# Kernel optimization log

Hardware: AMD Instinct MI355X
Metric: run time of the kernel (lower is better)

The kernel has to match this reference:

```python
import jax, jax.numpy as jnp
import numpy as np

B, S, D, NB = 8, 8192, 512, 16


def _ln(x, g, b, eps=1e-5):
    m = jnp.mean(x, axis=-1, keepdims=True)
    v = jnp.var(x, axis=-1, keepdims=True)
    return (x - m) / jnp.sqrt(v + eps) * g + b


def setup_inputs() -> dict:
    key = jax.random.key(0)
    ks = jax.random.split(key, 12)
    s = 0.02
    f32 = jnp.float32
    return {
        "emb_input": jax.random.normal(ks[0], (B, S, D), f32),
        "dis_input": jax.random.normal(ks[1], (B, S, D), f32),
        "torsion": jax.random.normal(ks[2], (B, D), f32),
        "dis_unlocked": 1,
        "delay_steps": 3,
        # embodied selector + per-block params (stacked over NB blocks)
        "emb_sel_W": jax.random.normal(ks[3], (D, NB), f32) * s,
        "emb_sel_b": jnp.zeros((NB,), f32),
        "emb_ln_g": jnp.ones((NB, D), f32),
        "emb_ln_b": jnp.zeros((NB, D), f32),
        "emb_w1": jax.random.normal(ks[4], (NB, D, D), f32) * s,
        "emb_b1": jnp.zeros((NB, D), f32),
        "emb_w2": jax.random.normal(ks[5], (NB, D, D), f32) * s,
        "emb_b2": jnp.zeros((NB, D), f32),
        # disembodied selector + per-block params
        "dis_sel_W": jax.random.normal(ks[6], (D, NB), f32) * s,
        "dis_sel_b": jnp.zeros((NB,), f32),
        "dis_ln1_g": jnp.ones((NB, D), f32),
        "dis_ln1_b": jnp.zeros((NB, D), f32),
        "dis_attn_W": jax.random.normal(ks[7], (NB, D, D), f32) * s,
        "dis_attn_b": jnp.zeros((NB, D), f32),
        "dis_ln2_g": jnp.ones((NB, D), f32),
        "dis_ln2_b": jnp.zeros((NB, D), f32),
        "dis_ff1_W": jax.random.normal(ks[8], (NB, D, 2 * D), f32) * s,
        "dis_ff1_b": jnp.zeros((NB, 2 * D), f32),
        "dis_ff2_W": jax.random.normal(ks[9], (NB, 2 * D, D), f32) * s,
        "dis_ff2_b": jnp.zeros((NB, D), f32),
    }


def reference(emb_input, dis_input, torsion, dis_unlocked, delay_steps,
              emb_sel_W, emb_sel_b, emb_ln_g, emb_ln_b, emb_w1, emb_b1, emb_w2, emb_b2,
              dis_sel_W, dis_sel_b, dis_ln1_g, dis_ln1_b, dis_attn_W, dis_attn_b,
              dis_ln2_g, dis_ln2_b, dis_ff1_W, dis_ff1_b, dis_ff2_W, dis_ff2_b):
    # ---- embodied branch: sigmoid-gated top-2 routing (indices from batch elem 0)
    scores = jax.nn.sigmoid(jnp.mean(emb_input, axis=1) @ emb_sel_W + emb_sel_b)  # [B,NB]
    _, top = jax.lax.top_k(scores[0], 2)
    t_emb = 1.0 + torsion[:, None, :] * 0.1  # [B,1,D]
    h = emb_input
    for i in range(2):  # fixed top-2, unrolled; block params gathered dynamically
        idx = top[i]
        hn = _ln(h, emb_ln_g[idx], emb_ln_b[idx])
        hn = jnp.tanh(hn @ emb_w1[idx] + emb_b1[idx]) @ emb_w2[idx] + emb_b2[idx]
        h = h + hn * t_emb * 0.3
    emb_h = h

    # ---- disembodied branch (dis_unlocked is a static Python int)
    dis_h = None
    if dis_unlocked:
        delayed = jnp.mean(dis_input, axis=1)  # [B,D]; single-write buffer returns current mean
        dscores = jax.nn.sigmoid(delayed @ dis_sel_W + dis_sel_b)
        _, dtop = jax.lax.top_k(dscores[0], 2)
        t_dis = 1.0 + torsion[:, None, :] * 0.05
        dh = dis_input
        for i in range(2):
            idx = dtop[i]
            h1 = _ln(dh, dis_ln1_g[idx], dis_ln1_b[idx])
            h1 = h1 @ dis_attn_W[idx] + dis_attn_b[idx]
            h1 = (h1 + delayed[:, None, :] * 0.2) * t_dis
            hm = dh + h1 * 0.5
            h2 = _ln(hm, dis_ln2_g[idx], dis_ln2_b[idx])
            h2 = jax.nn.gelu(h2 @ dis_ff1_W[idx] + dis_ff1_b[idx], approximate=False)
            h2 = h2 @ dis_ff2_W[idx] + dis_ff2_b[idx]
            dh = hm + h2 * 0.5
        dis_h = dh
    return (emb_h, dis_h)
```

## Files before the change

kernel.cpp:

```cpp
#include <hip/hip_runtime.h>
#include <stdint.h>

#define B_  8
#define S_  8192
#define D_  512
#define NB_ 16
#define M_  (B_*S_)

typedef short bf16x8 __attribute__((ext_vector_type(8)));
typedef float f32x4  __attribute__((ext_vector_type(4)));

static __device__ __forceinline__ unsigned short f2bf(float f) {
  unsigned int u = __float_as_uint(f);
  u += 0x7fff + ((u >> 16) & 1);
  return (unsigned short)(u >> 16);
}

static __device__ __forceinline__ void async_copy16(const unsigned short* g,
                                                    unsigned short* l) {
  auto* g1 = reinterpret_cast<const __attribute__((address_space(1))) uint32_t*>(
      reinterpret_cast<uintptr_t>(g));
  auto* l3 = reinterpret_cast<__attribute__((address_space(3))) uint32_t*>(
      reinterpret_cast<uintptr_t>(l));
  __builtin_amdgcn_global_load_lds(g1, l3, 16, 0, 0);
}

__global__ __launch_bounds__(256) void zero_kernel(float* p, int n) {
  int i = blockIdx.x * 256 + threadIdx.x;
  if (i < n) p[i] = 0.f;
}

__global__ __launch_bounds__(512) void colmean_kernel(const float* __restrict__ x,
                                                      float* __restrict__ acc) {
  int b = blockIdx.x, d = threadIdx.x;
  const float* p = x + ((size_t)b * S_ + (size_t)blockIdx.y * 512) * D_ + d;
  float s = 0.f;
  #pragma unroll 8
  for (int i = 0; i < 512; i++) s += p[(size_t)i * D_];
  atomicAdd(&acc[b * D_ + d], s);
}

__global__ __launch_bounds__(128) void top2_kernel(const float* __restrict__ embAcc,
                                                   const float* __restrict__ embW,
                                                   const float* __restrict__ embB,
                                                   const float* __restrict__ disAcc,
                                                   const float* __restrict__ disW,
                                                   const float* __restrict__ disB,
                                                   int* __restrict__ out) {
  int wave = threadIdx.x >> 6, lane = threadIdx.x & 63;
  const float* acc = wave ? disAcc : embAcc;
  const float* W   = wave ? disW   : embW;
  const float* bb  = wave ? disB   : embB;
  const float invS = 1.f / (float)S_;
  float logit[NB_];
  for (int nb = 0; nb < NB_; nb++) {
    float s = 0.f;
    for (int d = lane; d < D_; d += 64) s += acc[d] * invS * W[d * NB_ + nb];
    for (int o = 32; o; o >>= 1) s += __shfl_xor(s, o);
    logit[nb] = s + bb[nb];
  }
  if (lane == 0) {
    int i0 = 0;
    for (int i = 1; i < NB_; i++) if (logit[i] > logit[i0]) i0 = i;
    int i1 = (i0 == 0) ? 1 : 0;
    for (int i = 0; i < NB_; i++) if (i != i0 && logit[i] > logit[i1]) i1 = i;
    out[wave * 2 + 0] = i0;
    out[wave * 2 + 1] = i1;
  }
}

__global__ __launch_bounds__(256) void ln_cast_kernel(const float* __restrict__ x,
                                                      const float* __restrict__ gB,
                                                      const float* __restrict__ bB,
                                                      const int* __restrict__ idxPtr,
                                                      unsigned short* __restrict__ out) {
  int row  = blockIdx.x * 4 + (threadIdx.x >> 6);
  int lane = threadIdx.x & 63;
  const float4* xr = (const float4*)(x + (size_t)row * D_ + lane * 8);
  float4 v0 = xr[0], v1 = xr[1];
  float s  = v0.x + v0.y + v0.z + v0.w + v1.x + v1.y + v1.z + v1.w;
  float sq = v0.x*v0.x + v0.y*v0.y + v0.z*v0.z + v0.w*v0.w
           + v1.x*v1.x + v1.y*v1.y + v1.z*v1.z + v1.w*v1.w;
  for (int o = 32; o; o >>= 1) { s += __shfl_xor(s, o); sq += __shfl_xor(sq, o); }
  float mean = s * (1.f / D_);
  float var  = sq * (1.f / D_) - mean * mean;
  float rstd = rsqrtf(var + 1e-5f);
  int idx = *idxPtr;
  const float4* g4 = (const float4*)(gB + (size_t)idx * D_ + lane * 8);
  const float4* b4 = (const float4*)(bB + (size_t)idx * D_ + lane * 8);
  float4 g0 = g4[0], g1 = g4[1], c0 = b4[0], c1 = b4[1];
  float xv[8] = {v0.x, v0.y, v0.z, v0.w, v1.x, v1.y, v1.z, v1.w};
  float gv[8] = {g0.x, g0.y, g0.z, g0.w, g1.x, g1.y, g1.z, g1.w};
  float bv[8] = {c0.x, c0.y, c0.z, c0.w, c1.x, c1.y, c1.z, c1.w};
  unsigned short o8[8] __attribute__((aligned(16)));
  #pragma unroll
  for (int k = 0; k < 8; k++) o8[k] = f2bf((xv[k] - mean) * rstd * gv[k] + bv[k]);
  *(uint4*)(out + (size_t)row * D_ + lane * 8) = *(const uint4*)o8;
}

__global__ __launch_bounds__(256) void wconvert_kernel(const float* __restrict__ srcAll,
                                                       const int* __restrict__ idxPtr,
                                                       int K, int N,
                                                       unsigned short* __restrict__ dst) {
  __shared__ float t[32][33];
  int idx = *idxPtr;
  const float* src = srcAll + (size_t)idx * K * N;
  int k0 = blockIdx.y * 32, n0 = blockIdx.x * 32;
  int tid = threadIdx.x;
  int kl = tid >> 5, nl = tid & 31;
  #pragma unroll
  for (int r = 0; r < 4; r++)
    t[kl + r * 8][nl] = src[(size_t)(k0 + kl + r * 8) * N + n0 + nl];
  __syncthreads();
  #pragma unroll
  for (int r = 0; r < 4; r++)
    dst[(size_t)(n0 + kl + r * 8) * K + k0 + nl] = f2bf(t[nl][kl + r * 8]);
}

template<int EPI>
__global__ __launch_bounds__(256) void gemm_kernel(const unsigned short* __restrict__ A,
                                                   const unsigned short* __restrict__ Bt,
                                                   int K, int N,
                                                   const int* __restrict__ idxPtr,
                                                   const float* __restrict__ biasBase,
                                                   const float* __restrict__ hin,
                                                   float* __restrict__ fout,
                                                   unsigned short* __restrict__ bout,
                                                   const float* __restrict__ torsion,
                                                   const float* __restrict__ dAcc) {
  __shared__ __align__(16) unsigned short As[128 * 32];
  __shared__ __align__(16) unsigned short Bs[128 * 32];
  const int tid  = threadIdx.x;
  const int wave = tid >> 6, lane = tid & 63;
  const int quad = lane >> 4, l16 = lane & 15;
  const int wm = (wave >> 1) * 64, wn = (wave & 1) * 64;

  const int nT  = N >> 7;
  const int lgn = (nT == 4) ? 2 : 3;
  const int perX = gridDim.x >> 3;
  const int tile = (blockIdx.x & 7) * perX + (blockIdx.x >> 3);
  const int m0 = (tile >> lgn) * 128;
  const int n0 = (tile & (nT - 1)) * 128;

  const int lrow  = lane >> 2;
  const int segSw = (((lane & 3) ^ ((lane >> 3) & 3)) * 8);
  const unsigned short* AgLo = A  + (size_t)(m0 + wave * 16 + lrow) * K + segSw;
  const unsigned short* AgHi = AgLo + (size_t)64 * K;
  const unsigned short* BgLo = Bt + (size_t)(n0 + wave * 16 + lrow) * K + segSw;
  const unsigned short* BgHi = BgLo + (size_t)64 * K;
  unsigned short* AsLo = &As[(wave * 16) * 32];
  unsigned short* AsHi = &As[(wave * 16 + 64) * 32];
  unsigned short* BsLo = &Bs[(wave * 16) * 32];
  unsigned short* BsHi = &Bs[(wave * 16 + 64) * 32];

  const int rsw = (l16 >> 1) & 3;

  f32x4 acc[4][4] = {};
  for (int kt = 0; kt < K; kt += 32) {
    async_copy16(AgLo + kt, AsLo);
    async_copy16(AgHi + kt, AsHi);
    async_copy16(BgLo + kt, BsLo);
    async_copy16(BgHi + kt, BsHi);
    __syncthreads();
    bf16x8 af[4], bfr[4];
    #pragma unroll
    for (int i = 0; i < 4; i++)
      af[i] = *(const bf16x8*)(&As[(size_t)(wm + i * 16 + l16) * 32 + (quad ^ rsw) * 8]);
    #pragma unroll
    for (int j = 0; j < 4; j++)
      bfr[j] = *(const bf16x8*)(&Bs[(size_t)(wn + j * 16 + l16) * 32 + (quad ^ rsw) * 8]);
    #pragma unroll
    for (int i = 0; i < 4; i++)
      #pragma unroll
      for (int j = 0; j < 4; j++)
        acc[i][j] = __builtin_amdgcn_mfma_f32_16x16x32_bf16(af[i], bfr[j], acc[i][j], 0, 0, 0);
    __syncthreads();
  }

  const int idx = *idxPtr;
  const float* bias = biasBase + (size_t)idx * N;
  const float invS = 1.f / (float)S_;
  #pragma unroll
  for (int i = 0; i < 4; i++) {
    int rowb = m0 + wm + i * 16 + quad * 4;
    #pragma unroll
    for (int j = 0; j < 4; j++) {
      int col = n0 + wn + j * 16 + l16;
      float bc = bias[col];
      #pragma unroll
      for (int r = 0; r < 4; r++) {
        int row = rowb + r;
        size_t off = (size_t)row * N + col;
        float v = acc[i][j][r] + bc;
        if constexpr (EPI == 0) {
          bout[off] = f2bf(tanhf(v));
        } else if constexpr (EPI == 1) {
          int b = row >> 13;
          float t = 1.f + 0.1f * torsion[b * D_ + col];
          fout[off] = hin[off] + v * t * 0.3f;
        } else if constexpr (EPI == 2) {
          int b = row >> 13;
          float t = 1.f + 0.05f * torsion[b * D_ + col];
          float h1 = (v + 0.2f * dAcc[b * D_ + col] * invS) * t;
          fout[off] = hin[off] + 0.5f * h1;
        } else if constexpr (EPI == 3) {
          float gl = 0.5f * v * (1.f + erff(v * 0.70710678118654752f));
          bout[off] = f2bf(gl);
        } else {
          fout[off] = hin[off] + 0.5f * v;
        }
      }
    }
  }
}

extern "C" void kernel_launch(void* const* d_in, const int* in_sizes, int n_in,
                              void* d_out, int out_size, void* d_ws, size_t ws_size,
                              hipStream_t stream) {
  const float* emb_input  = (const float*)d_in[0];
  const float* dis_input  = (const float*)d_in[1];
  const float* torsion    = (const float*)d_in[2];
  const float* emb_sel_W  = (const float*)d_in[5];
  const float* emb_sel_b  = (const float*)d_in[6];
  const float* emb_ln_g   = (const float*)d_in[7];
  const float* emb_ln_b   = (const float*)d_in[8];
  const float* emb_w1     = (const float*)d_in[9];
  const float* emb_b1     = (const float*)d_in[10];
  const float* emb_w2     = (const float*)d_in[11];
  const float* emb_b2     = (const float*)d_in[12];
  const float* dis_sel_W  = (const float*)d_in[13];
  const float* dis_sel_b  = (const float*)d_in[14];
  const float* dis_ln1_g  = (const float*)d_in[15];
  const float* dis_ln1_b  = (const float*)d_in[16];
  const float* dis_attn_W = (const float*)d_in[17];
  const float* dis_attn_b = (const float*)d_in[18];
  const float* dis_ln2_g  = (const float*)d_in[19];
  const float* dis_ln2_b  = (const float*)d_in[20];
  const float* dis_ff1_W  = (const float*)d_in[21];
  const float* dis_ff1_b  = (const float*)d_in[22];
  const float* dis_ff2_W  = (const float*)d_in[23];
  const float* dis_ff2_b  = (const float*)d_in[24];

  char* w = (char*)d_ws;
  float* accE = (float*)w;
  float* accD = (float*)(w + 16384);
  int*   top  = (int*)(w + 32768);
  size_t o = 33024;
  unsigned short* w1t   = (unsigned short*)(w + o); o += 524288;
  unsigned short* w2t   = (unsigned short*)(w + o); o += 524288;
  unsigned short* attnT = (unsigned short*)(w + o); o += 524288;
  unsigned short* ff1T  = (unsigned short*)(w + o); o += 1048576;
  unsigned short* ff2T  = (unsigned short*)(w + o); o += 1048576;
  unsigned short* Abuf  = (unsigned short*)(w + o); o += (size_t)M_ * D_ * 2;
  unsigned short* T1    = (unsigned short*)(w + o); o += (size_t)M_ * D_ * 2;

  float* outEmb = (float*)d_out;
  float* outDis = outEmb + (size_t)M_ * D_;
  unsigned short* Gbuf = (unsigned short*)d_out;

  zero_kernel<<<32, 256, 0, stream>>>(accE, 2 * B_ * D_);
  colmean_kernel<<<dim3(1, 16), 512, 0, stream>>>(emb_input, accE);
  colmean_kernel<<<dim3(8, 16), 512, 0, stream>>>(dis_input, accD);
  top2_kernel<<<1, 128, 0, stream>>>(accE, emb_sel_W, emb_sel_b,
                                     accD, dis_sel_W, dis_sel_b, top);

  for (int s = 0; s < 2; s++) {
    const int* di = top + 2 + s;
    const float* dh = (s == 0) ? dis_input : outDis;
    wconvert_kernel<<<dim3(16, 16), 256, 0, stream>>>(dis_attn_W, di, 512, 512, attnT);
    wconvert_kernel<<<dim3(32, 16), 256, 0, stream>>>(dis_ff1_W,  di, 512, 1024, ff1T);
    wconvert_kernel<<<dim3(16, 32), 256, 0, stream>>>(dis_ff2_W,  di, 1024, 512, ff2T);
    ln_cast_kernel<<<M_ / 4, 256, 0, stream>>>(dh, dis_ln1_g, dis_ln1_b, di, Abuf);
    gemm_kernel<2><<<2048, 256, 0, stream>>>(Abuf, attnT, 512, 512, di,
        dis_attn_b, dh, outDis, nullptr, torsion, accD);
    ln_cast_kernel<<<M_ / 4, 256, 0, stream>>>(outDis, dis_ln2_g, dis_ln2_b, di, Abuf);
    gemm_kernel<3><<<4096, 256, 0, stream>>>(Abuf, ff1T, 512, 1024, di,
        dis_ff1_b, nullptr, nullptr, Gbuf, nullptr, nullptr);
    gemm_kernel<4><<<2048, 256, 0, stream>>>(Gbuf, ff2T, 1024, 512, di,
        dis_ff2_b, outDis, outDis, nullptr, nullptr, nullptr);
  }

  for (int s = 0; s < 2; s++) {
    const int* ei = top + s;
    const float* h = (s == 0) ? emb_input : outEmb;
    wconvert_kernel<<<dim3(16, 16), 256, 0, stream>>>(emb_w1, ei, 512, 512, w1t);
    wconvert_kernel<<<dim3(16, 16), 256, 0, stream>>>(emb_w2, ei, 512, 512, w2t);
    ln_cast_kernel<<<M_ / 4, 256, 0, stream>>>(h, emb_ln_g, emb_ln_b, ei, Abuf);
    gemm_kernel<0><<<2048, 256, 0, stream>>>(Abuf, w1t, 512, 512, ei,
        emb_b1, nullptr, nullptr, T1, nullptr, nullptr);
    gemm_kernel<1><<<2048, 256, 0, stream>>>(T1, w2t, 512, 512, ei,
        emb_b2, h, outEmb, nullptr, torsion, nullptr);
  }
}
```

Measured before the change: 1.791 ms.

## Enlarge GEMM tiles to 256x256 with a 4-stage async LDS pipeline

Rewrites the bf16 MFMA GEMM to use 512-thread blocks that each compute a 256x256 output tile. K-slices are staged through a 4-deep ring of LDS buffers via async global-to-LDS copies, with explicit vmcnt waits and barriers so loads overlap compute. s_setprio is raised around the MFMA bursts. The goal is more data reuse per tile and less time stalled on loads and barriers. In exchange it drops the old LDS XOR swizzle, which risks bank conflicts, uses 128 KB of LDS per block, which limits occupancy, and issues redundant wrap-around prefetches on the last iterations.

```diff
diff --git a/kernel.cpp b/kernel.cpp
--- a/kernel.cpp
+++ b/kernel.cpp
@@ -118,80 +118,106 @@
 }
 
 template<int EPI>
-__global__ __launch_bounds__(256) void gemm_kernel(const unsigned short* __restrict__ A,
-                                                   const unsigned short* __restrict__ Bt,
-                                                   int K, int N,
-                                                   const int* __restrict__ idxPtr,
-                                                   const float* __restrict__ biasBase,
-                                                   const float* __restrict__ hin,
-                                                   float* __restrict__ fout,
-                                                   unsigned short* __restrict__ bout,
-                                                   const float* __restrict__ torsion,
-                                                   const float* __restrict__ dAcc) {
-  __shared__ __align__(16) unsigned short As[128 * 32];
-  __shared__ __align__(16) unsigned short Bs[128 * 32];
+__global__ __launch_bounds__(512, 2) void gemm_kernel(const unsigned short* __restrict__ A,
+                                                      const unsigned short* __restrict__ Bt,
+                                                      int K, int N,
+                                                      const int* __restrict__ idxPtr,
+                                                      const float* __restrict__ biasBase,
+                                                      const float* __restrict__ hin,
+                                                      float* __restrict__ fout,
+                                                      unsigned short* __restrict__ bout,
+                                                      const float* __restrict__ torsion,
+                                                      const float* __restrict__ dAcc) {
+  __shared__ __align__(16) unsigned short lds[4][2][8192];
   const int tid  = threadIdx.x;
-  const int wave = tid >> 6, lane = tid & 63;
+  const int wid  = tid >> 6, lane = tid & 63;
   const int quad = lane >> 4, l16 = lane & 15;
-  const int wm = (wave >> 1) * 64, wn = (wave & 1) * 64;
-
-  const int nT  = N >> 7;
-  const int lgn = (nT == 4) ? 2 : 3;
+  const int wr = wid >> 2, wc = wid & 3;
+
+  const int nT  = N >> 8;
+  const int lgn = (nT == 2) ? 1 : 2;
   const int perX = gridDim.x >> 3;
-  const int tile = (blockIdx.x & 7) * perX + (blockIdx.x >> 3);
-  const int m0 = (tile >> lgn) * 128;
-  const int n0 = (tile & (nT - 1)) * 128;
-
-  const int lrow  = lane >> 2;
-  const int segSw = (((lane & 3) ^ ((lane >> 3) & 3)) * 8);
-  const unsigned short* AgLo = A  + (size_t)(m0 + wave * 16 + lrow) * K + segSw;
-  const unsigned short* AgHi = AgLo + (size_t)64 * K;
-  const unsigned short* BgLo = Bt + (size_t)(n0 + wave * 16 + lrow) * K + segSw;
-  const unsigned short* BgHi = BgLo + (size_t)64 * K;
-  unsigned short* AsLo = &As[(wave * 16) * 32];
-  unsigned short* AsHi = &As[(wave * 16 + 64) * 32];
-  unsigned short* BsLo = &Bs[(wave * 16) * 32];
-  unsigned short* BsHi = &Bs[(wave * 16 + 64) * 32];
-
-  const int rsw = (l16 >> 1) & 3;
-
-  f32x4 acc[4][4] = {};
-  for (int kt = 0; kt < K; kt += 32) {
-    async_copy16(AgLo + kt, AsLo);
-    async_copy16(AgHi + kt, AsHi);
-    async_copy16(BgLo + kt, BsLo);
-    async_copy16(BgHi + kt, BsHi);
-    __syncthreads();
+  const int tile = ((int)blockIdx.x & 7) * perX + ((int)blockIdx.x >> 3);
+  const int m0 = (tile >> lgn) << 8;
+  const int n0 = (tile & (nT - 1)) << 8;
+
+  const int srow = tid >> 2;
+  const int scol = (tid & 3) * 8;
+  const unsigned short* Ag0 = A  + (size_t)(m0 + srow) * K + scol;
+  const unsigned short* Ag1 = Ag0 + (size_t)128 * K;
+  const unsigned short* Bg0 = Bt + (size_t)(n0 + srow) * K + scol;
+  const unsigned short* Bg1 = Bg0 + (size_t)128 * K;
+
+  auto stageA = [&](int kt, int b) {
+    async_copy16(Ag0 + (size_t)kt * 32, &lds[b][0][tid * 8]);
+    async_copy16(Ag1 + (size_t)kt * 32, &lds[b][0][4096 + tid * 8]);
+  };
+  auto stageB = [&](int kt, int b) {
+    async_copy16(Bg0 + (size_t)kt * 32, &lds[b][1][tid * 8]);
+    async_copy16(Bg1 + (size_t)kt * 32, &lds[b][1][4096 + tid * 8]);
+  };
+
+  f32x4 acc[8][4] = {};
+  const int nK = K >> 5;
+
+  stageA(0, 0); stageB(0, 0);
+  stageA(1, 1); stageB(1, 1);
+  stageA(2, 2); stageB(2, 2);
+
+  const int aoff = (wr * 128 + l16) * 32 + quad * 8;
+  const int boff = (wc * 64  + l16) * 32 + quad * 8;
+
+  for (int k = 0; k < nK; ++k) {
+    const int cur = k & 3;
+    const int nxt = (k + 3) & 3;
+    const int kn  = (k + 3 < nK) ? (k + 3) : 0;
+    stageA(kn, nxt);
+    asm volatile("s_waitcnt vmcnt(10)" ::: "memory");
+    asm volatile("s_barrier" ::: "memory");
+
+    const unsigned short* Ab = &lds[cur][0][aoff];
+    const unsigned short* Bb = &lds[cur][1][boff];
     bf16x8 af[4], bfr[4];
     #pragma unroll
-    for (int i = 0; i < 4; i++)
-      af[i] = *(const bf16x8*)(&As[(size_t)(wm + i * 16 + l16) * 32 + (quad ^ rsw) * 8]);
-    #pragma unroll
-    for (int j = 0; j < 4; j++)
-      bfr[j] = *(const bf16x8*)(&Bs[(size_t)(wn + j * 16 + l16) * 32 + (quad ^ rsw) * 8]);
-    #pragma unroll
-    for (int i = 0; i < 4; i++)
+    for (int i = 0; i < 4; ++i) af[i]  = *(const bf16x8*)(Ab + i * 512);
+    #pragma unroll
+    for (int j = 0; j < 4; ++j) bfr[j] = *(const bf16x8*)(Bb + j * 512);
+    __builtin_amdgcn_s_setprio(1);
+    #pragma unroll
+    for (int i = 0; i < 4; ++i)
       #pragma unroll
-      for (int j = 0; j < 4; j++)
+      for (int j = 0; j < 4; ++j)
         acc[i][j] = __builtin_amdgcn_mfma_f32_16x16x32_bf16(af[i], bfr[j], acc[i][j], 0, 0, 0);
-    __syncthreads();
+    __builtin_amdgcn_s_setprio(0);
+
+    stageB(kn, nxt);
+    #pragma unroll
+    for (int i = 0; i < 4; ++i) af[i] = *(const bf16x8*)(Ab + (64 + i * 16) * 32);
+    __builtin_amdgcn_s_setprio(1);
+    #pragma unroll
+    for (int i = 0; i < 4; ++i)
+      #pragma unroll
+      for (int j = 0; j < 4; ++j)
+        acc[4 + i][j] = __builtin_amdgcn_mfma_f32_16x16x32_bf16(af[i], bfr[j], acc[4 + i][j], 0, 0, 0);
+    __builtin_amdgcn_s_setprio(0);
+    asm volatile("s_barrier" ::: "memory");
   }
 
   const int idx = *idxPtr;
   const float* bias = biasBase + (size_t)idx * N;
   const float invS = 1.f / (float)S_;
   #pragma unroll
-  for (int i = 0; i < 4; i++) {
-    int rowb = m0 + wm + i * 16 + quad * 4;
-    #pragma unroll
-    for (int j = 0; j < 4; j++) {
-      int col = n0 + wn + j * 16 + l16;
+  for (int mf = 0; mf < 8; ++mf) {
+    int rowb = m0 + wr * 128 + mf * 16 + quad * 4;
+    #pragma unroll
+    for (int nf = 0; nf < 4; ++nf) {
+      int col = n0 + wc * 64 + nf * 16 + l16;
       float bc = bias[col];
       #pragma unroll
-      for (int r = 0; r < 4; r++) {
+      for (int r = 0; r < 4; ++r) {
         int row = rowb + r;
         size_t off = (size_t)row * N + col;
-        float v = acc[i][j][r] + bc;
+        float v = acc[mf][nf][r] + bc;
         if constexpr (EPI == 0) {
           bout[off] = f2bf(tanhf(v));
         } else if constexpr (EPI == 1) {
@@ -212,6 +238,7 @@
       }
     }
   }
+  asm volatile("s_waitcnt vmcnt(0)" ::: "memory");
 }
 
 extern "C" void kernel_launch(void* const* d_in, const int* in_sizes, int n_in,
@@ -271,12 +298,12 @@
     wconvert_kernel<<<dim3(32, 16), 256, 0, stream>>>(dis_ff1_W,  di, 512, 1024, ff1T);
     wconvert_kernel<<<dim3(16, 32), 256, 0, stream>>>(dis_ff2_W,  di, 1024, 512, ff2T);
     ln_cast_kernel<<<M_ / 4, 256, 0, stream>>>(dh, dis_ln1_g, dis_ln1_b, di, Abuf);
-    gemm_kernel<2><<<2048, 256, 0, stream>>>(Abuf, attnT, 512, 512, di,
+    gemm_kernel<2><<<512, 512, 0, stream>>>(Abuf, attnT, 512, 512, di,
         dis_attn_b, dh, outDis, nullptr, torsion, accD);
     ln_cast_kernel<<<M_ / 4, 256, 0, stream>>>(outDis, dis_ln2_g, dis_ln2_b, di, Abuf);
-    gemm_kernel<3><<<4096, 256, 0, stream>>>(Abuf, ff1T, 512, 1024, di,
+    gemm_kernel<3><<<1024, 512, 0, stream>>>(Abuf, ff1T, 512, 1024, di,
         dis_ff1_b, nullptr, nullptr, Gbuf, nullptr, nullptr);
-    gemm_kernel<4><<<2048, 256, 0, stream>>>(Gbuf, ff2T, 1024, 512, di,
+    gemm_kernel<4><<<512, 512, 0, stream>>>(Gbuf, ff2T, 1024, 512, di,
         dis_ff2_b, outDis, outDis, nullptr, nullptr, nullptr);
   }
 
@@ -286,9 +313,9 @@
     wconvert_kernel<<<dim3(16, 16), 256, 0, stream>>>(emb_w1, ei, 512, 512, w1t);
     wconvert_kernel<<<dim3(16, 16), 256, 0, stream>>>(emb_w2, ei, 512, 512, w2t);
     ln_cast_kernel<<<M_ / 4, 256, 0, stream>>>(h, emb_ln_g, emb_ln_b, ei, Abuf);
-    gemm_kernel<0><<<2048, 256, 0, stream>>>(Abuf, w1t, 512, 512, ei,
+    gemm_kernel<0><<<512, 512, 0, stream>>>(Abuf, w1t, 512, 512, ei,
         emb_b1, nullptr, nullptr, T1, nullptr, nullptr);
-    gemm_kernel<1><<<2048, 256, 0, stream>>>(T1, w2t, 512, 512, ei,
+    gemm_kernel<1><<<512, 512, 0, stream>>>(T1, w2t, 512, 512, ei,
         emb_b2, h, outEmb, nullptr, torsion, nullptr);
   }
 }
```

Result: faster. 1.662 ms (-7.2%).

## Triple-buffer GEMM LDS loads with async prefetch and use fast tanh/GELU

Applied to the files above, without the earlier changes.

The GEMM main loop moves from a single LDS buffer with two full barriers per K-step to a three-slot ring. Global-to-LDS async copies are issued two tiles ahead and gated with a partial vmcnt wait, so loads can overlap the MFMAs. It also raises MFMA priority with s_setprio and sets an occupancy hint of 3 blocks per CU. The epilogue swaps tanhf and erff for exp/rcp-based approximations (Abramowitz-Stegun erf), which costs some accuracy but stays well within bf16 output precision.

```diff
diff --git a/kernel.cpp b/kernel.cpp
--- a/kernel.cpp
+++ b/kernel.cpp
@@ -14,6 +14,22 @@
   unsigned int u = __float_as_uint(f);
   u += 0x7fff + ((u >> 16) & 1);
   return (unsigned short)(u >> 16);
+}
+
+static __device__ __forceinline__ float fast_gelu(float v) {
+  float x = fabsf(v) * 0.70710678118654752f;
+  float t = __builtin_amdgcn_rcpf(1.f + 0.3275911f * x);
+  float poly = ((((1.061405429f * t - 1.453152027f) * t + 1.421413741f) * t
+                 - 0.284496736f) * t + 0.254829592f) * t;
+  float erfx = 1.f - poly * __expf(-x * x);
+  return 0.5f * v * (1.f + copysignf(erfx, v));
+}
+
+static __device__ __forceinline__ float fast_tanh(float v) {
+  float a = fabsf(v);
+  float e = __expf(2.f * a);
+  float r = 1.f - 2.f * __builtin_amdgcn_rcpf(e + 1.f);
+  return copysignf(r, v);
 }
 
 static __device__ __forceinline__ void async_copy16(const unsigned short* g,
@@ -118,82 +134,95 @@
 }
 
 template<int EPI>
-__global__ __launch_bounds__(256) void gemm_kernel(const unsigned short* __restrict__ A,
-                                                   const unsigned short* __restrict__ Bt,
-                                                   int K, int N,
-                                                   const int* __restrict__ idxPtr,
-                                                   const float* __restrict__ biasBase,
-                                                   const float* __restrict__ hin,
-                                                   float* __restrict__ fout,
-                                                   unsigned short* __restrict__ bout,
-                                                   const float* __restrict__ torsion,
-                                                   const float* __restrict__ dAcc) {
-  __shared__ __align__(16) unsigned short As[128 * 32];
-  __shared__ __align__(16) unsigned short Bs[128 * 32];
+__global__ __launch_bounds__(256, 3) void gemm_kernel(const unsigned short* __restrict__ A,
+                                                      const unsigned short* __restrict__ Bt,
+                                                      int K, int N,
+                                                      const int* __restrict__ idxPtr,
+                                                      const float* __restrict__ biasBase,
+                                                      const float* __restrict__ hin,
+                                                      float* __restrict__ fout,
+                                                      unsigned short* __restrict__ bout,
+                                                      const float* __restrict__ torsion,
+                                                      const float* __restrict__ dAcc) {
+  __shared__ __align__(16) unsigned short lds[3][2][4096];
   const int tid  = threadIdx.x;
-  const int wave = tid >> 6, lane = tid & 63;
+  const int wid  = tid >> 6, lane = tid & 63;
   const int quad = lane >> 4, l16 = lane & 15;
-  const int wm = (wave >> 1) * 64, wn = (wave & 1) * 64;
+  const int wm = (wid >> 1) * 64, wn = (wid & 1) * 64;
 
   const int nT  = N >> 7;
   const int lgn = (nT == 4) ? 2 : 3;
   const int perX = gridDim.x >> 3;
-  const int tile = (blockIdx.x & 7) * perX + (blockIdx.x >> 3);
-  const int m0 = (tile >> lgn) * 128;
-  const int n0 = (tile & (nT - 1)) * 128;
-
-  const int lrow  = lane >> 2;
-  const int segSw = (((lane & 3) ^ ((lane >> 3) & 3)) * 8);
-  const unsigned short* AgLo = A  + (size_t)(m0 + wave * 16 + lrow) * K + segSw;
-  const unsigned short* AgHi = AgLo + (size_t)64 * K;
-  const unsigned short* BgLo = Bt + (size_t)(n0 + wave * 16 + lrow) * K + segSw;
-  const unsigned short* BgHi = BgLo + (size_t)64 * K;
-  unsigned short* AsLo = &As[(wave * 16) * 32];
-  unsigned short* AsHi = &As[(wave * 16 + 64) * 32];
-  unsigned short* BsLo = &Bs[(wave * 16) * 32];
-  unsigned short* BsHi = &Bs[(wave * 16 + 64) * 32];
-
-  const int rsw = (l16 >> 1) & 3;
+  const int tile = ((int)blockIdx.x & 7) * perX + ((int)blockIdx.x >> 3);
+  const int m0 = (tile >> lgn) << 7;
+  const int n0 = (tile & (nT - 1)) << 7;
+
+  const int srow = tid >> 2;
+  const int scol = (((tid & 3) ^ ((tid >> 3) & 3)) * 8);
+  const unsigned short* Ag0 = A  + (size_t)(m0 + srow) * K + scol;
+  const unsigned short* Ag1 = Ag0 + (size_t)64 * K;
+  const unsigned short* Bg0 = Bt + (size_t)(n0 + srow) * K + scol;
+  const unsigned short* Bg1 = Bg0 + (size_t)64 * K;
+
+  auto stage = [&](int kt, int slot) {
+    async_copy16(Ag0 + (size_t)kt * 32, &lds[slot][0][tid * 8]);
+    async_copy16(Ag1 + (size_t)kt * 32, &lds[slot][0][2048 + tid * 8]);
+    async_copy16(Bg0 + (size_t)kt * 32, &lds[slot][1][tid * 8]);
+    async_copy16(Bg1 + (size_t)kt * 32, &lds[slot][1][2048 + tid * 8]);
+  };
 
   f32x4 acc[4][4] = {};
-  for (int kt = 0; kt < K; kt += 32) {
-    async_copy16(AgLo + kt, AsLo);
-    async_copy16(AgHi + kt, AsHi);
-    async_copy16(BgLo + kt, BsLo);
-    async_copy16(BgHi + kt, BsHi);
-    __syncthreads();
+  const int nK = K >> 5;
+
+  stage(0, 0);
+  stage(1, 1);
+
+  const int rsw  = (l16 >> 1) & 3;
+  const int aoff = (wm + l16) * 32 + ((quad ^ rsw) * 8);
+  const int boff = (wn + l16) * 32 + ((quad ^ rsw) * 8);
+
+  for (int k = 0; k < nK; ++k) {
+    const int cur = k % 3;
+    const int nxt = (k + 2) % 3;
+    const int kn  = (k + 2 < nK) ? (k + 2) : 0;
+    stage(kn, nxt);
+    asm volatile("s_waitcnt vmcnt(8)" ::: "memory");
+    asm volatile("s_barrier" ::: "memory");
+
+    const unsigned short* Ab = &lds[cur][0][aoff];
+    const unsigned short* Bb = &lds[cur][1][boff];
     bf16x8 af[4], bfr[4];
     #pragma unroll
-    for (int i = 0; i < 4; i++)
-      af[i] = *(const bf16x8*)(&As[(size_t)(wm + i * 16 + l16) * 32 + (quad ^ rsw) * 8]);
+    for (int i = 0; i < 4; ++i) af[i]  = *(const bf16x8*)(Ab + i * 512);
     #pragma unroll
-    for (int j = 0; j < 4; j++)
-      bfr[j] = *(const bf16x8*)(&Bs[(size_t)(wn + j * 16 + l16) * 32 + (quad ^ rsw) * 8]);
+    for (int j = 0; j < 4; ++j) bfr[j] = *(const bf16x8*)(Bb + j * 512);
+    __builtin_amdgcn_s_setprio(1);
     #pragma unroll
-    for (int i = 0; i < 4; i++)
+    for (int i = 0; i < 4; ++i)
       #pragma unroll
-      for (int j = 0; j < 4; j++)
+      for (int j = 0; j < 4; ++j)
         acc[i][j] = __builtin_amdgcn_mfma_f32_16x16x32_bf16(af[i], bfr[j], acc[i][j], 0, 0, 0);
-    __syncthreads();
+    __builtin_amdgcn_s_setprio(0);
+    asm volatile("s_barrier" ::: "memory");
   }
 
   const int idx = *idxPtr;
   const float* bias = biasBase + (size_t)idx * N;
   const float invS = 1.f / (float)S_;
   #pragma unroll
-  for (int i = 0; i < 4; i++) {
+  for (int i = 0; i < 4; ++i) {
     int rowb = m0 + wm + i * 16 + quad * 4;
     #pragma unroll
-    for (int j = 0; j < 4; j++) {
+    for (int j = 0; j < 4; ++j) {
       int col = n0 + wn + j * 16 + l16;
       float bc = bias[col];
       #pragma unroll
-      for (int r = 0; r < 4; r++) {
+      for (int r = 0; r < 4; ++r) {
         int row = rowb + r;
         size_t off = (size_t)row * N + col;
         float v = acc[i][j][r] + bc;
         if constexpr (EPI == 0) {
-          bout[off] = f2bf(tanhf(v));
+          bout[off] = f2bf(fast_tanh(v));
         } else if constexpr (EPI == 1) {
           int b = row >> 13;
           float t = 1.f + 0.1f * torsion[b * D_ + col];
@@ -204,14 +233,14 @@
           float h1 = (v + 0.2f * dAcc[b * D_ + col] * invS) * t;
           fout[off] = hin[off] + 0.5f * h1;
         } else if constexpr (EPI == 3) {
-          float gl = 0.5f * v * (1.f + erff(v * 0.70710678118654752f));
-          bout[off] = f2bf(gl);
+          bout[off] = f2bf(fast_gelu(v));
         } else {
           fout[off] = hin[off] + 0.5f * v;
         }
       }
     }
   }
+  asm volatile("s_waitcnt vmcnt(0)" ::: "memory");
 }
 
 extern "C" void kernel_launch(void* const* d_in, const int* in_sizes, int n_in,
```

Result: faster. 1.598 ms (-10.7%).
